# Kernel optimization log

Hardware: AMD Instinct MI355X
Metric: run time of the kernel (lower is better)

The kernel has to match this reference:

```python
import jax, jax.numpy as jnp
import numpy as np

B, T, H = 2, 2048, 1024
I = 4096            # intermediate dim
HEADS = 4
RET = 128           # private expert retrieval dim
NUM_EXPERTS = 4096
NUM_KEYS = 64       # sqrt(NUM_EXPERTS)
K = 8               # num_cdmmoe_experts_per_head


def setup_inputs() -> dict:
    key = jax.random.key(0)
    ks = jax.random.split(key, 7)
    return {
        "hidden_states": jax.random.normal(ks[0], (B, T, H), jnp.float32),
        "W_up": jax.random.normal(ks[1], (I, H), jnp.float32) * 0.02,
        "W_down": jax.random.normal(ks[2], (H, I), jnp.float32) * 0.02,
        "W_q": jax.random.normal(ks[3], (HEADS * RET, H), jnp.float32) * 0.02,
        "keys": jax.random.normal(ks[4], (HEADS, NUM_KEYS, 2, RET // 2), jnp.float32) * 0.02,
        "down_embed": jax.random.normal(ks[5], (NUM_EXPERTS, H), jnp.float32) * 0.02,
        "up_embed": jax.random.normal(ks[6], (NUM_EXPERTS, H), jnp.float32) * 0.02,
    }


def reference(hidden_states, W_up, W_down, W_q, keys, down_embed, up_embed):
    b, t, hd = hidden_states.shape
    h, nk, _, n = keys.shape  # heads, num_keys, 2, half retrieval dim
    # queries: [b,t,h*2n] -> [2,b,t,h,n]
    q = jnp.einsum('btd,ed->bte', hidden_states, W_q)
    q = q.reshape(b, t, 2, h, n).transpose(2, 0, 1, 3, 4)
    # product-key similarities: [2,b,t,h,num_keys]
    sim = jnp.einsum('pbthn,hkpn->pbthk', q, keys)
    scores_xy, idx_xy = jax.lax.top_k(sim, K)  # [2,b,t,h,K]
    sx, sy = scores_xy[0], scores_xy[1]
    ix, iy = idx_xy[0], idx_xy[1]
    # cartesian combine: [b,t,h,K*K]
    all_scores = (sx[..., :, None] + sy[..., None, :]).reshape(b, t, h, K * K)
    all_idx = (ix[..., :, None] * nk + iy[..., None, :]).reshape(b, t, h, K * K)
    scores, pk = jax.lax.top_k(all_scores, K)               # [b,t,h,K]
    indices = jnp.take_along_axis(all_idx, pk, axis=-1)     # [b,t,h,K]
    de = down_embed[indices]  # [b,t,h,K,H]
    ue = up_embed[indices]    # [b,t,h,K,H]
    w = jax.nn.silu(jnp.einsum('btd,bthkd->bthk', hidden_states, de)
                    * jax.nn.softmax(scores, axis=-1))
    experts_states = jnp.einsum('bthk,bthkd->btd', w, ue)
    dense = jnp.einsum('bti,di->btd', jax.nn.silu(jnp.einsum('btd,id->bti', hidden_states, W_up)), W_down)
    return dense + experts_states
```

## Files before the change

### kernel.cpp

```cpp
#include <hip/hip_runtime.h>

typedef unsigned short u16;
typedef unsigned int u32;

#define TOKENS 4096
#define HDIM 1024
#define IDIM 4096
#define NHEADS 4
#define NKEYS 64
#define TOPK 8
#define QDIM 512

typedef __bf16 bf16x8 __attribute__((ext_vector_type(8)));
typedef float  f32x4  __attribute__((ext_vector_type(4)));
typedef u16    u16x8  __attribute__((ext_vector_type(8)));
typedef u16    u16x4  __attribute__((ext_vector_type(4)));
typedef u32    u32x4  __attribute__((ext_vector_type(4)));

__device__ __forceinline__ u16 f2bf(float f) {
    u32 u = __float_as_uint(f);
    u += 0x7fffu + ((u >> 16) & 1u);
    return (u16)(u >> 16);
}
__device__ __forceinline__ float bf2f(u16 h) { return __uint_as_float(((u32)h) << 16); }

#define H_N4   1048576
#define WUP_N4 1048576
#define WDN_N4 1048576
#define DE_N4  1048576
#define UE_N4  1048576
#define CVT_TOT (H_N4 + WUP_N4 + WDN_N4 + DE_N4 + UE_N4)

__device__ __forceinline__ void cvt1(const float* in, u16* hi, u16* lo, int i) {
    float4 v = reinterpret_cast<const float4*>(in)[i];
    float vf[4] = {v.x, v.y, v.z, v.w};
    ushort4 h;
    u16 hh[4];
#pragma unroll
    for (int j = 0; j < 4; j++) hh[j] = f2bf(vf[j]);
    h.x = hh[0]; h.y = hh[1]; h.z = hh[2]; h.w = hh[3];
    reinterpret_cast<ushort4*>(hi)[i] = h;
    if (lo) {
        ushort4 l4;
        u16 ll[4];
#pragma unroll
        for (int j = 0; j < 4; j++) ll[j] = f2bf(vf[j] - bf2f(hh[j]));
        l4.x = ll[0]; l4.y = ll[1]; l4.z = ll[2]; l4.w = ll[3];
        reinterpret_cast<ushort4*>(lo)[i] = l4;
    }
}

__device__ __forceinline__ void cvt1_f8(const float* in, u32* out8, int i) {
    float4 v = reinterpret_cast<const float4*>(in)[i];
    u32 w = __builtin_amdgcn_cvt_pk_fp8_f32(v.x, v.y, 0u, false);
    w = __builtin_amdgcn_cvt_pk_fp8_f32(v.z, v.w, w, true);
    out8[i] = w;
}

__global__ __launch_bounds__(256) void cvt_all(
    const float* __restrict__ hidden, const float* __restrict__ W_up,
    const float* __restrict__ W_down, const float* __restrict__ de,
    const float* __restrict__ ue,
    u16* __restrict__ hid_hi, u16* __restrict__ hid_lo,
    u16* __restrict__ wup, u16* __restrict__ wdn,
    u32* __restrict__ de_f8, u32* __restrict__ ue_f8) {
    int i = blockIdx.x * 256 + threadIdx.x;
    if (i >= CVT_TOT) return;
    if (i < H_N4) { cvt1(hidden, hid_hi, hid_lo, i); return; }
    i -= H_N4;
    if (i < WUP_N4) { cvt1(W_up, wup, nullptr, i); return; }
    i -= WUP_N4;
    if (i < WDN_N4) { cvt1(W_down, wdn, nullptr, i); return; }
    i -= WDN_N4;
    if (i < DE_N4) { cvt1_f8(de, de_f8, i); return; }
    i -= DE_N4;
    cvt1_f8(ue, ue_f8, i);
}

__global__ __launch_bounds__(256) void weff_kernel(
    const float* __restrict__ keys, const float* __restrict__ Wq,
    u16* __restrict__ weff_hi, u16* __restrict__ weff_lo) {
    __shared__ float kk[64][65];
    __shared__ float wq_s[64][128];

    const int g = blockIdx.x >> 3, ds = blockIdx.x & 7;
    const int p = g >> 2, h = g & 3;
    const int d0 = ds * 128;
    const int t = threadIdx.x;
    const int base = p * 256 + h * 64;

    {
        int k = t >> 2, part = t & 3;
        const float* krow = keys + (((size_t)(h * NKEYS + k) * 2 + p) * 64);
#pragma unroll
        for (int j = 0; j < 4; j++) {
            int n0 = part * 16 + j * 4;
            float4 v = *reinterpret_cast<const float4*>(krow + n0);
            kk[k][n0 + 0] = v.x; kk[k][n0 + 1] = v.y;
            kk[k][n0 + 2] = v.z; kk[k][n0 + 3] = v.w;
        }
    }
    {
        int n = t >> 2, dpart = t & 3;
        const float* wrow = Wq + (size_t)(base + n) * HDIM + d0;
#pragma unroll
        for (int j = 0; j < 8; j++) {
            int dd = dpart * 32 + j * 4;
            float4 v = *reinterpret_cast<const float4*>(wrow + dd);
            *reinterpret_cast<float4*>(&wq_s[n][dd]) = v;
        }
    }
    __syncthreads();

    const int k = t & 63, dq = t >> 6;
    float acc[32];
#pragma unroll
    for (int i = 0; i < 32; i++) acc[i] = 0.f;
    for (int n = 0; n < 64; n++) {
        float kv = kk[k][n];
        const float4* wrow = reinterpret_cast<const float4*>(&wq_s[n][dq * 32]);
#pragma unroll
        for (int j = 0; j < 8; j++) {
            float4 w4 = wrow[j];
            acc[j * 4 + 0] += kv * w4.x; acc[j * 4 + 1] += kv * w4.y;
            acc[j * 4 + 2] += kv * w4.z; acc[j * 4 + 3] += kv * w4.w;
        }
    }
    size_t ro = (size_t)(g * 64 + k) * HDIM + d0 + dq * 32;
#pragma unroll
    for (int j = 0; j < 8; j++) {
        ushort4 hh, ll;
        u16 hv[4], lv[4];
#pragma unroll
        for (int i = 0; i < 4; i++) {
            float a = acc[j * 4 + i];
            hv[i] = f2bf(a);
            lv[i] = f2bf(a - bf2f(hv[i]));
        }
        hh.x = hv[0]; hh.y = hv[1]; hh.z = hv[2]; hh.w = hv[3];
        ll.x = lv[0]; ll.y = lv[1]; ll.z = lv[2]; ll.w = lv[3];
        *reinterpret_cast<ushort4*>(weff_hi + ro + j * 4) = hh;
        *reinterpret_cast<ushort4*>(weff_lo + ro + j * 4) = ll;
    }
}

__global__ __launch_bounds__(256) void reduce_add(float* __restrict__ out,
                                                  const float* __restrict__ p, int n4) {
    int i = blockIdx.x * 256 + threadIdx.x;
    if (i >= n4) return;
    float4 a = reinterpret_cast<const float4*>(out)[i];
    float4 b = reinterpret_cast<const float4*>(p)[i];
    a.x += b.x; a.y += b.y; a.z += b.z; a.w += b.w;
    reinterpret_cast<float4*>(out)[i] = a;
}

__device__ __forceinline__ void gload16(const void* g, void* s) {
    auto gp = reinterpret_cast<const __attribute__((address_space(1))) u32*>(
        reinterpret_cast<uintptr_t>(g));
    auto sp = reinterpret_cast<__attribute__((address_space(3))) u32*>(
        reinterpret_cast<uintptr_t>(s));
    __builtin_amdgcn_global_load_lds(gp, sp, 16, 0, 0);
}

#define BK 32

__device__ __forceinline__ int swz(int a) { return a ^ (((a >> 7) & 3) << 4); }

template <int ROWS, int THREADS>
__device__ __forceinline__ void stage_tile(const u16* g, size_t krow_b, size_t kb0,
                                           u16* s, int t) {
#pragma unroll
    for (int rnd = 0; rnd < ROWS * 64 / (THREADS * 16); rnd++) {
        int o = t * 16 + rnd * THREADS * 16;
        int os = swz(o);
        int row = o >> 6, kb = os & 63;
        gload16((const char*)g + (size_t)row * krow_b + kb0 + kb, (char*)s + o);
    }
}

template <int EPI, int TBM, int TBN, int WVM, int WVN, bool SPLIT, int KCHUNKS, bool XSWZ>
__global__ __launch_bounds__(WVM * WVN * 64) void gemm_bt(
    const u16* __restrict__ A, const u16* __restrict__ Alo,
    const u16* __restrict__ B, const u16* __restrict__ Blo,
    void* __restrict__ Cout, void* __restrict__ Cout2,
    const float* __restrict__ ext, int M, int N, int K) {
    constexpr int THREADS = WVM * WVN * 64;
    constexpr int NS = SPLIT ? 2 : 1;
    constexpr int WM = TBM / WVM, WN = TBN / WVN;
    constexpr int FM = WM / 16, FN = WN / 16;
    constexpr int ASZ = NS * TBM * BK;
    constexpr int BSZ = NS * TBN * BK;
    __shared__ u16 As[2][ASZ];
    __shared__ u16 Bs[2][BSZ];
    const int t = threadIdx.x;
    const int lane = t & 63;
    const int wave = t >> 6;
    const int wr = wave / WVN, wc = wave % WVN;

    int bx = blockIdx.x, by = blockIdx.y;
    if (XSWZ) {
        int gx = gridDim.x, gy = gridDim.y;
        int n = gx * gy;
        int bid = by * gx + bx;
        int q = n >> 3;
        bid = (bid & 7) * q + (bid >> 3);
        bx = bid % gx; by = bid / gx;
    }
    const int m0 = by * TBM;
    const int n0 = bx * TBN;
    const int klen = K / KCHUNKS;
    const int koff = (KCHUNKS > 1) ? blockIdx.z * klen : 0;

    f32x4 acc[FM][FN];
#pragma unroll
    for (int i = 0; i < FM; i++)
#pragma unroll
        for (int j = 0; j < FN; j++) acc[i][j] = (f32x4){0.f, 0.f, 0.f, 0.f};

    const size_t krow = (size_t)K * 2;
    const int ro = lane & 15;
    const int ko = (lane >> 4) * 16;

    const u16* Ab = A + (size_t)m0 * K;
    const u16* Bb = B + (size_t)n0 * K;
    const u16* Alb = SPLIT ? Alo + (size_t)m0 * K : nullptr;
    const u16* Blb = SPLIT ? Blo + (size_t)n0 * K : nullptr;

    auto stage_all = [&](int b, int k0) {
        size_t kb0 = (size_t)k0 * 2;
        stage_tile<TBM, THREADS>(Ab, krow, kb0, As[b], t);
        stage_tile<TBN, THREADS>(Bb, krow, kb0, Bs[b], t);
        if (SPLIT) {
            stage_tile<TBM, THREADS>(Alb, krow, kb0, As[b] + TBM * BK, t);
            stage_tile<TBN, THREADS>(Blb, krow, kb0, Bs[b] + TBN * BK, t);
        }
    };

    stage_all(0, koff);
    __syncthreads();
    int cur = 0;

    for (int k0 = koff; k0 < koff + klen; k0 += BK) {
        if (k0 + BK < koff + klen) stage_all(cur ^ 1, k0 + BK);
        const u16* Ac = As[cur];
        const u16* Bc = Bs[cur];
        bf16x8 fa[FM], fb[FN], fal[FM], fbl[FN];
#pragma unroll
        for (int i = 0; i < FM; i++) {
            int a = swz((wr * WM + i * 16 + ro) * 64 + ko);
            fa[i] = *reinterpret_cast<const bf16x8*>((const char*)Ac + a);
            if (SPLIT)
                fal[i] = *reinterpret_cast<const bf16x8*>((const char*)(Ac + TBM * BK) + a);
        }
#pragma unroll
        for (int j = 0; j < FN; j++) {
            int a = swz((wc * WN + j * 16 + ro) * 64 + ko);
            fb[j] = *reinterpret_cast<const bf16x8*>((const char*)Bc + a);
            if (SPLIT)
                fbl[j] = *reinterpret_cast<const bf16x8*>((const char*)(Bc + TBN * BK) + a);
        }
#pragma unroll
        for (int i = 0; i < FM; i++)
#pragma unroll
            for (int j = 0; j < FN; j++) {
                acc[i][j] = __builtin_amdgcn_mfma_f32_16x16x32_bf16(fa[i], fb[j],
                                                                    acc[i][j], 0, 0, 0);
                if (SPLIT) {
                    acc[i][j] = __builtin_amdgcn_mfma_f32_16x16x32_bf16(fa[i], fbl[j],
                                                                        acc[i][j], 0, 0, 0);
                    acc[i][j] = __builtin_amdgcn_mfma_f32_16x16x32_bf16(fal[i], fb[j],
                                                                        acc[i][j], 0, 0, 0);
                }
            }
        __syncthreads();
        cur ^= 1;
    }

#pragma unroll
    for (int i = 0; i < FM; i++)
#pragma unroll
        for (int j = 0; j < FN; j++) {
            int col = n0 + wc * WN + j * 16 + (lane & 15);
            int rbase = m0 + wr * WM + i * 16 + (lane >> 4) * 4;
#pragma unroll
            for (int r = 0; r < 4; r++) {
                int row = rbase + r;
                float v = acc[i][j][r];
                size_t off = (size_t)row * N + col;
                if (EPI == 0) {
                    ((float*)Cout)[off] = v;
                } else if (EPI == 1) {
                    float s = v / (1.f + __expf(-v));
                    ((u16*)Cout)[off] = f2bf(s);
                } else {
                    if (KCHUNKS == 1 || blockIdx.z == 0)
                        ((float*)Cout)[off] = v + ext[off];
                    else
                        ((float*)Cout2)[off] = v;
                }
            }
        }
}

__device__ __forceinline__ int rank64(const float* base, float v, int l) {
    const float4* gv = reinterpret_cast<const float4*>(base);
    int rank = 0;
#pragma unroll
    for (int n = 0; n < 16; n++) {
        float4 o = gv[n];
        int b = n * 4;
        rank += (o.x > v) || (o.x == v && (b + 0) < l);
        rank += (o.y > v) || (o.y == v && (b + 1) < l);
        rank += (o.z > v) || (o.z == v && (b + 2) < l);
        rank += (o.w > v) || (o.w == v && (b + 3) < l);
    }
    return rank;
}

__global__ __launch_bounds__(512) void router(
    const float* __restrict__ Simb,
    int* __restrict__ sidx_g, float* __restrict__ gate_g) {
    __shared__ float sims[QDIM];
    __shared__ float topv[8][TOPK];
    __shared__ int topi[8][TOPK];
    __shared__ float pv[NHEADS][64];
    __shared__ float st8[NHEADS][TOPK];
    __shared__ int sid8[NHEADS][TOPK];

    const int tok = blockIdx.x;
    const int tid = threadIdx.x;
    const int w = tid >> 6, l = tid & 63;

    sims[tid] = Simb[(size_t)tok * QDIM + tid];
    __syncthreads();

    {
        float v = sims[w * 64 + l];
        int rank = rank64(sims + w * 64, v, l);
        if (rank < TOPK) { topv[w][rank] = v; topi[w][rank] = l; }
    }
    __syncthreads();

    if (w < NHEADS) {
        pv[w][l] = topv[w][l >> 3] + topv[4 + w][l & 7];
    }
    __syncthreads();

    if (w < NHEADS) {
        float v = pv[w][l];
        int rank = rank64(pv[w], v, l);
        if (rank < TOPK) {
            st8[w][rank] = v;
            sid8[w][rank] = topi[w][l >> 3] * NKEYS + topi[4 + w][l & 7];
        }
    }
    __syncthreads();

    if (tid < NHEADS * TOPK) {
        int h = tid >> 3, r = tid & 7;
        float m0 = st8[h][0];
        float s = 0.f;
#pragma unroll
        for (int i = 0; i < TOPK; i++) s += __expf(st8[h][i] - m0);
        size_t o = ((size_t)tok * NHEADS + h) * TOPK + r;
        sidx_g[o] = sid8[h][r];
        gate_g[o] = __expf(st8[h][r] - m0) / s;
    }
}

__global__ __launch_bounds__(256) void expert_gather(
    const u16* __restrict__ hid_bf, const u32* __restrict__ de_f8,
    const u32* __restrict__ ue_f8, const int* __restrict__ sidx_g,
    const float* __restrict__ gate_g, float* __restrict__ expst) {
    __shared__ float wks[32];
    __shared__ int eids_s[32];

    const int tok = blockIdx.x;
    const int w = threadIdx.x >> 6, l = threadIdx.x & 63;

    {
        u16x8 hv[2];
        const u16* hrow = hid_bf + (size_t)tok * HDIM + l * 16;
        hv[0] = *reinterpret_cast<const u16x8*>(hrow);
        hv[1] = *reinterpret_cast<const u16x8*>(hrow + 8);
        float h16[16];
#pragma unroll
        for (int t2 = 0; t2 < 8; t2++) { h16[t2] = bf2f(hv[0][t2]); h16[8 + t2] = bf2f(hv[1][t2]); }
        int eid[8];
        float gt[8];
#pragma unroll
        for (int j = 0; j < 8; j++) {
            size_t o = (size_t)tok * 32 + w * 8 + j;
            eid[j] = sidx_g[o];
            gt[j] = gate_g[o];
        }
        u32x4 dv[8];
#pragma unroll
        for (int j = 0; j < 8; j++) {
            const u32x4* dr = reinterpret_cast<const u32x4*>(de_f8 + (size_t)eid[j] * 256 + l * 4);
            dv[j] = *dr;
        }
        float dot[8];
#pragma unroll
        for (int j = 0; j < 8; j++) {
            float s = 0.f;
#pragma unroll
            for (int w2 = 0; w2 < 4; w2++) {
                u32 word = dv[j][w2];
                s += h16[w2 * 4 + 0] * __builtin_amdgcn_cvt_f32_fp8(word, 0);
                s += h16[w2 * 4 + 1] * __builtin_amdgcn_cvt_f32_fp8(word, 1);
                s += h16[w2 * 4 + 2] * __builtin_amdgcn_cvt_f32_fp8(word, 2);
                s += h16[w2 * 4 + 3] * __builtin_amdgcn_cvt_f32_fp8(word, 3);
            }
            dot[j] = s;
        }
#pragma unroll
        for (int m = 32; m; m >>= 1)
#pragma unroll
            for (int j = 0; j < 8; j++) dot[j] += __shfl_xor(dot[j], m, 64);
#pragma unroll
        for (int j = 0; j < 8; j++)
            if (l == j) {
                float x = dot[j] * gt[j];
                wks[w * 8 + j] = x / (1.f + __expf(-x));
                eids_s[w * 8 + j] = eid[j];
            }
    }
    __syncthreads();

    {
        float acc0 = 0.f, acc1 = 0.f, acc2 = 0.f, acc3 = 0.f;
        const u32* ubase = ue_f8 + w * 64 + l;
#pragma unroll
        for (int m = 0; m < 32; m++) {
            int e = eids_s[m];
            float wk = wks[m];
            u32 u = ubase[(size_t)e * 256];
            acc0 += wk * __builtin_amdgcn_cvt_f32_fp8(u, 0);
            acc1 += wk * __builtin_amdgcn_cvt_f32_fp8(u, 1);
            acc2 += wk * __builtin_amdgcn_cvt_f32_fp8(u, 2);
            acc3 += wk * __builtin_amdgcn_cvt_f32_fp8(u, 3);
        }
        float4 a4 = make_float4(acc0, acc1, acc2, acc3);
        *reinterpret_cast<float4*>(expst + (size_t)tok * HDIM + w * 256 + l * 4) = a4;
    }
}

extern "C" void kernel_launch(void* const* d_in, const int* in_sizes, int n_in,
                              void* d_out, int out_size, void* d_ws, size_t ws_size,
                              hipStream_t stream) {
    const float* hidden = (const float*)d_in[0];
    const float* W_up = (const float*)d_in[1];
    const float* W_down = (const float*)d_in[2];
    const float* W_q = (const float*)d_in[3];
    const float* keys = (const float*)d_in[4];
    const float* down_embed = (const float*)d_in[5];
    const float* up_embed = (const float*)d_in[6];
    float* out = (float*)d_out;

    char* ws = (char*)d_ws;
    size_t off = 0;
    auto alloc = [&](size_t bytes) {
        void* p = ws + off;
        off += (bytes + 255) & ~(size_t)255;
        return p;
    };
    u16* hid_hi = (u16*)alloc((size_t)TOKENS * HDIM * 2);
    u16* hid_lo = (u16*)alloc((size_t)TOKENS * HDIM * 2);
    float* Simb = (float*)alloc((size_t)TOKENS * QDIM * 4);
    float* partial = (float*)hid_lo;
    u16* weff_hi = (u16*)alloc((size_t)QDIM * HDIM * 2);
    u16* weff_lo = (u16*)alloc((size_t)QDIM * HDIM * 2);
    u16* wup = (u16*)alloc((size_t)IDIM * HDIM * 2);
    u16* wdn = (u16*)alloc((size_t)HDIM * IDIM * 2);
    u16* act = (u16*)alloc((size_t)TOKENS * IDIM * 2);
    u32* de_f8 = (u32*)alloc((size_t)4096 * HDIM);
    u32* ue_f8 = (u32*)alloc((size_t)4096 * HDIM);
    float* expst = (float*)alloc((size_t)TOKENS * HDIM * 4);
    int* sidx_g = (int*)alloc((size_t)TOKENS * 32 * 4);
    float* gate_g = (float*)alloc((size_t)TOKENS * 32 * 4);

    cvt_all<<<(CVT_TOT + 255) / 256, 256, 0, stream>>>(
        hidden, W_up, W_down, down_embed, up_embed,
        hid_hi, hid_lo, wup, wdn, de_f8, ue_f8);
    weff_kernel<<<64, 256, 0, stream>>>(keys, W_q, weff_hi, weff_lo);

    gemm_bt<0, 64, 128, 2, 2, true, 1, false>
        <<<dim3(QDIM / 128, TOKENS / 64), 256, 0, stream>>>(
        hid_hi, hid_lo, weff_hi, weff_lo, Simb, nullptr, nullptr, TOKENS, QDIM, HDIM);

    router<<<TOKENS, 512, 0, stream>>>(Simb, sidx_g, gate_g);
    expert_gather<<<TOKENS, 256, 0, stream>>>(hid_hi, de_f8, ue_f8, sidx_g, gate_g, expst);

    gemm_bt<1, 256, 128, 4, 2, false, 1, true>
        <<<dim3(IDIM / 128, TOKENS / 256), 512, 0, stream>>>(
        hid_hi, nullptr, wup, nullptr, act, nullptr, nullptr, TOKENS, IDIM, HDIM);
    gemm_bt<2, 128, 128, 2, 2, false, 2, true>
        <<<dim3(HDIM / 128, TOKENS / 128, 2), 256, 0, stream>>>(
        act, nullptr, wdn, nullptr, out, partial, expst, TOKENS, HDIM, IDIM);
    reduce_add<<<(TOKENS * HDIM / 4 + 255) / 256, 256, 0, stream>>>(out, partial,
                                                                    TOKENS * HDIM / 4);
}
```

Measured before the change: 222.7 us.

## Add 256x256-tile pipelined GEMM for dense MLP with four-way split-K down projection

Replaces the generic GEMM used for the dense up and down projections with a dedicated 512-thread kernel. It uses 256x256 output tiles and a K-step of 64, and splits each K-step into four quadrant phases that interleave direct-to-LDS loads with MFMA, using manual waitcnt, barriers and setprio. The down projection is split four ways along K; the partial sums go to reused workspace buffers, and a three-input reduction kernel adds them into the output. The goal is more data reuse per tile and better overlap of loads with compute. In exchange the kernel needs more registers (one block per CU), and correctness depends on aliasing partial buffers onto workspace that is dead by that point.

```diff
diff --git a/kernel.cpp b/kernel.cpp
--- a/kernel.cpp
+++ b/kernel.cpp
@@ -144,13 +144,18 @@
     }
 }
 
-__global__ __launch_bounds__(256) void reduce_add(float* __restrict__ out,
-                                                  const float* __restrict__ p, int n4) {
+__global__ __launch_bounds__(256) void reduce_add3(float* __restrict__ out,
+                                                   const float* __restrict__ p1,
+                                                   const float* __restrict__ p2,
+                                                   const float* __restrict__ p3, int n4) {
     int i = blockIdx.x * 256 + threadIdx.x;
     if (i >= n4) return;
     float4 a = reinterpret_cast<const float4*>(out)[i];
-    float4 b = reinterpret_cast<const float4*>(p)[i];
-    a.x += b.x; a.y += b.y; a.z += b.z; a.w += b.w;
+    float4 b = reinterpret_cast<const float4*>(p1)[i];
+    float4 c = reinterpret_cast<const float4*>(p2)[i];
+    float4 d = reinterpret_cast<const float4*>(p3)[i];
+    a.x += b.x + c.x + d.x; a.y += b.y + c.y + d.y;
+    a.z += b.z + c.z + d.z; a.w += b.w + c.w + d.w;
     reinterpret_cast<float4*>(out)[i] = a;
 }
 
@@ -178,12 +183,11 @@
     }
 }
 
-template <int EPI, int TBM, int TBN, int WVM, int WVN, bool SPLIT, int KCHUNKS, bool XSWZ>
+template <int EPI, int TBM, int TBN, int WVM, int WVN, bool SPLIT>
 __global__ __launch_bounds__(WVM * WVN * 64) void gemm_bt(
     const u16* __restrict__ A, const u16* __restrict__ Alo,
     const u16* __restrict__ B, const u16* __restrict__ Blo,
-    void* __restrict__ Cout, void* __restrict__ Cout2,
-    const float* __restrict__ ext, int M, int N, int K) {
+    void* __restrict__ Cout, int M, int N, int K) {
     constexpr int THREADS = WVM * WVN * 64;
     constexpr int NS = SPLIT ? 2 : 1;
     constexpr int WM = TBM / WVM, WN = TBN / WVN;
@@ -196,20 +200,8 @@
     const int lane = t & 63;
     const int wave = t >> 6;
     const int wr = wave / WVN, wc = wave % WVN;
-
-    int bx = blockIdx.x, by = blockIdx.y;
-    if (XSWZ) {
-        int gx = gridDim.x, gy = gridDim.y;
-        int n = gx * gy;
-        int bid = by * gx + bx;
-        int q = n >> 3;
-        bid = (bid & 7) * q + (bid >> 3);
-        bx = bid % gx; by = bid / gx;
-    }
-    const int m0 = by * TBM;
-    const int n0 = bx * TBN;
-    const int klen = K / KCHUNKS;
-    const int koff = (KCHUNKS > 1) ? blockIdx.z * klen : 0;
+    const int m0 = blockIdx.y * TBM;
+    const int n0 = blockIdx.x * TBN;
 
     f32x4 acc[FM][FN];
 #pragma unroll
@@ -236,12 +228,12 @@
         }
     };
 
-    stage_all(0, koff);
+    stage_all(0, 0);
     __syncthreads();
     int cur = 0;
 
-    for (int k0 = koff; k0 < koff + klen; k0 += BK) {
-        if (k0 + BK < koff + klen) stage_all(cur ^ 1, k0 + BK);
+    for (int k0 = 0; k0 < K; k0 += BK) {
+        if (k0 + BK < K) stage_all(cur ^ 1, k0 + BK);
         const u16* Ac = As[cur];
         const u16* Bc = Bs[cur];
         bf16x8 fa[FM], fb[FN], fal[FM], fbl[FN];
@@ -284,22 +276,151 @@
             int rbase = m0 + wr * WM + i * 16 + (lane >> 4) * 4;
 #pragma unroll
             for (int r = 0; r < 4; r++) {
-                int row = rbase + r;
-                float v = acc[i][j][r];
-                size_t off = (size_t)row * N + col;
-                if (EPI == 0) {
-                    ((float*)Cout)[off] = v;
-                } else if (EPI == 1) {
+                size_t off = (size_t)(rbase + r) * N + col;
+                ((float*)Cout)[off] = acc[i][j][r];
+            }
+        }
+}
+
+template <int EPI, int KCHUNKS>
+__global__ __launch_bounds__(512, 1) void gemm8(
+    const u16* __restrict__ A, const u16* __restrict__ B,
+    void* __restrict__ Cout,
+    float* __restrict__ P1, float* __restrict__ P2, float* __restrict__ P3,
+    const float* __restrict__ ext, int M, int N, int K) {
+    __shared__ u16 As[2][2][128 * 64];
+    __shared__ u16 Bs[2][2][128 * 64];
+    const int t = threadIdx.x;
+    const int lane = t & 63;
+    const int wave = t >> 6;
+    const int wr = wave >> 2, wc = wave & 3;
+    const int ro = lane & 15;
+    const int ko = (lane >> 4) * 16;
+
+    int bx = blockIdx.x, by = blockIdx.y;
+    {
+        int gx = gridDim.x;
+        int n = gx * gridDim.y;
+        int bid = by * gx + bx;
+        int q = n >> 3;
+        bid = (bid & 7) * q + (bid >> 3);
+        bx = bid % gx; by = bid / gx;
+    }
+    const int m0 = by * 256, n0 = bx * 256;
+    const int klen = K / KCHUNKS;
+    const int z = (KCHUNKS > 1) ? blockIdx.z : 0;
+    const int koff = z * klen;
+    const int NT = klen / 64;
+
+    const size_t krowB = (size_t)K * 2;
+    const u16* A0p = A + (size_t)m0 * K;
+    const u16* A1p = A + (size_t)(m0 + 128) * K;
+    const u16* B0p = B + (size_t)n0 * K;
+    const u16* B1p = B + (size_t)(n0 + 128) * K;
+
+    f32x4 acc[8][4];
+#pragma unroll
+    for (int i = 0; i < 8; i++)
+#pragma unroll
+        for (int j = 0; j < 4; j++) acc[i][j] = (f32x4){0.f, 0.f, 0.f, 0.f};
+
+    auto stage = [&](const u16* gbase, int kelem, u16* lds) {
+#pragma unroll
+        for (int rnd = 0; rnd < 2; rnd++) {
+            int o = t * 16 + rnd * 8192;
+            int os = o ^ (((o >> 7) & 7) << 4);
+            int row = o >> 7, kb = os & 127;
+            gload16((const char*)gbase + (size_t)row * krowB + (size_t)kelem * 2 + kb,
+                    (char*)lds + o);
+        }
+    };
+
+    stage(A0p, koff, As[0][0]);
+    stage(B0p, koff, Bs[0][0]);
+    stage(B1p, koff, Bs[0][1]);
+    stage(A1p, koff, As[0][1]);
+    stage(A0p, koff + 64, As[1][0]);
+    stage(B0p, koff + 64, Bs[1][0]);
+    asm volatile("s_waitcnt vmcnt(4)" ::: "memory");
+    asm volatile("s_barrier" ::: "memory");
+
+#define PHASE(R)                                                               \
+    {                                                                          \
+        const int qm = (R) >> 1, qn = (R) & 1;                                 \
+        const u16* Ah = As[u & 1][qm];                                         \
+        const u16* Bh = Bs[u & 1][qn];                                         \
+        bf16x8 fa[4][2], fb[2][2];                                             \
+        _Pragma("unroll") for (int i = 0; i < 4; i++) {                        \
+            int hr = wr * 64 + i * 16 + ro;                                    \
+            int sw = (hr & 7) << 4;                                            \
+            _Pragma("unroll") for (int kk = 0; kk < 2; kk++)                   \
+                fa[i][kk] = *reinterpret_cast<const bf16x8*>(                  \
+                    (const char*)Ah + ((hr * 128 + kk * 64 + ko) ^ sw));       \
+        }                                                                      \
+        _Pragma("unroll") for (int j = 0; j < 2; j++) {                        \
+            int hr = wc * 32 + j * 16 + ro;                                    \
+            int sw = (hr & 7) << 4;                                            \
+            _Pragma("unroll") for (int kk = 0; kk < 2; kk++)                   \
+                fb[j][kk] = *reinterpret_cast<const bf16x8*>(                  \
+                    (const char*)Bh + ((hr * 128 + kk * 64 + ko) ^ sw));       \
+        }                                                                      \
+        if ((R) == 0 && u + 1 < NT) stage(B1p, koff + (u + 1) * 64, Bs[(u + 1) & 1][1]); \
+        if ((R) == 1 && u + 1 < NT) stage(A1p, koff + (u + 1) * 64, As[(u + 1) & 1][1]); \
+        if ((R) == 2 && u + 2 < NT) stage(A0p, koff + (u + 2) * 64, As[u & 1][0]);       \
+        if ((R) == 3 && u + 2 < NT) stage(B0p, koff + (u + 2) * 64, Bs[u & 1][0]);       \
+        asm volatile("s_barrier" ::: "memory");                                \
+        __builtin_amdgcn_s_setprio(1);                                         \
+        _Pragma("unroll") for (int i = 0; i < 4; i++)                          \
+            _Pragma("unroll") for (int j = 0; j < 2; j++)                      \
+                _Pragma("unroll") for (int kk = 0; kk < 2; kk++)               \
+                    acc[qm * 4 + i][qn * 2 + j] =                              \
+                        __builtin_amdgcn_mfma_f32_16x16x32_bf16(               \
+                            fa[i][kk], fb[j][kk], acc[qm * 4 + i][qn * 2 + j], \
+                            0, 0, 0);                                          \
+        __builtin_amdgcn_s_setprio(0);                                         \
+        if ((R) == 3) {                                                        \
+            if (u == NT - 2)                                                   \
+                asm volatile("s_waitcnt vmcnt(0)" ::: "memory");               \
+            else                                                               \
+                asm volatile("s_waitcnt vmcnt(4)" ::: "memory");               \
+        }                                                                      \
+        asm volatile("s_barrier" ::: "memory");                                \
+    }
+
+    for (int u = 0; u < NT; ++u) {
+        PHASE(0)
+        PHASE(1)
+        PHASE(2)
+        PHASE(3)
+    }
+#undef PHASE
+
+#pragma unroll
+    for (int qi = 0; qi < 8; qi++) {
+#pragma unroll
+        for (int qj = 0; qj < 4; qj++) {
+            const int qm = qi >> 2, i = qi & 3;
+            const int qn = qj >> 1, j = qj & 1;
+            int row0 = m0 + qm * 128 + wr * 64 + i * 16 + (lane >> 4) * 4;
+            int col = n0 + qn * 128 + wc * 32 + j * 16 + ro;
+#pragma unroll
+            for (int r = 0; r < 4; r++) {
+                float v = acc[qi][qj][r];
+                size_t off = (size_t)(row0 + r) * N + col;
+                if (EPI == 1) {
                     float s = v / (1.f + __expf(-v));
                     ((u16*)Cout)[off] = f2bf(s);
                 } else {
-                    if (KCHUNKS == 1 || blockIdx.z == 0)
+                    if (z == 0)
                         ((float*)Cout)[off] = v + ext[off];
-                    else
-                        ((float*)Cout2)[off] = v;
+                    else {
+                        float* P = (z == 1) ? P1 : (z == 2) ? P2 : P3;
+                        P[off] = v;
+                    }
                 }
             }
         }
+    }
 }
 
 __device__ __forceinline__ int rank64(const float* base, float v, int l) {
@@ -468,7 +589,6 @@
     u16* hid_hi = (u16*)alloc((size_t)TOKENS * HDIM * 2);
     u16* hid_lo = (u16*)alloc((size_t)TOKENS * HDIM * 2);
     float* Simb = (float*)alloc((size_t)TOKENS * QDIM * 4);
-    float* partial = (float*)hid_lo;
     u16* weff_hi = (u16*)alloc((size_t)QDIM * HDIM * 2);
     u16* weff_lo = (u16*)alloc((size_t)QDIM * HDIM * 2);
     u16* wup = (u16*)alloc((size_t)IDIM * HDIM * 2);
@@ -479,25 +599,26 @@
     float* expst = (float*)alloc((size_t)TOKENS * HDIM * 4);
     int* sidx_g = (int*)alloc((size_t)TOKENS * 32 * 4);
     float* gate_g = (float*)alloc((size_t)TOKENS * 32 * 4);
+    float* P3 = (float*)alloc((size_t)TOKENS * HDIM * 4);
+    float* P1 = (float*)hid_hi;
+    float* P2 = (float*)Simb;
 
     cvt_all<<<(CVT_TOT + 255) / 256, 256, 0, stream>>>(
         hidden, W_up, W_down, down_embed, up_embed,
         hid_hi, hid_lo, wup, wdn, de_f8, ue_f8);
     weff_kernel<<<64, 256, 0, stream>>>(keys, W_q, weff_hi, weff_lo);
 
-    gemm_bt<0, 64, 128, 2, 2, true, 1, false>
+    gemm_bt<0, 64, 128, 2, 2, true>
         <<<dim3(QDIM / 128, TOKENS / 64), 256, 0, stream>>>(
-        hid_hi, hid_lo, weff_hi, weff_lo, Simb, nullptr, nullptr, TOKENS, QDIM, HDIM);
+        hid_hi, hid_lo, weff_hi, weff_lo, Simb, TOKENS, QDIM, HDIM);
 
     router<<<TOKENS, 512, 0, stream>>>(Simb, sidx_g, gate_g);
     expert_gather<<<TOKENS, 256, 0, stream>>>(hid_hi, de_f8, ue_f8, sidx_g, gate_g, expst);
 
-    gemm_bt<1, 256, 128, 4, 2, false, 1, true>
-        <<<dim3(IDIM / 128, TOKENS / 256), 512, 0, stream>>>(
-        hid_hi, nullptr, wup, nullptr, act, nullptr, nullptr, TOKENS, IDIM, HDIM);
-    gemm_bt<2, 128, 128, 2, 2, false, 2, true>
-        <<<dim3(HDIM / 128, TOKENS / 128, 2), 256, 0, stream>>>(
-        act, nullptr, wdn, nullptr, out, partial, expst, TOKENS, HDIM, IDIM);
-    reduce_add<<<(TOKENS * HDIM / 4 + 255) / 256, 256, 0, stream>>>(out, partial,
-                                                                    TOKENS * HDIM / 4);
-}
+    gemm8<1, 1><<<dim3(IDIM / 256, TOKENS / 256), 512, 0, stream>>>(
+        hid_hi, wup, act, nullptr, nullptr, nullptr, nullptr, TOKENS, IDIM, HDIM);
+    gemm8<2, 4><<<dim3(HDIM / 256, TOKENS / 256, 4), 512, 0, stream>>>(
+        act, wdn, out, P1, P2, P3, expst, TOKENS, HDIM, IDIM);
+    reduce_add3<<<(TOKENS * HDIM / 4 + 255) / 256, 256, 0, stream>>>(
+        out, P1, P2, P3, TOKENS * HDIM / 4);
+}
```

Result: slower. 246.3 us (+10.6%).

## Add triple-buffered GEMM with explicit vmcnt waits for dense up/down projections

Applied to the files above, without the earlier changes.

Introduces a new gemm_p3 kernel for the two dense MLP GEMMs that uses three LDS stages, prefetching two K-tiles ahead. It waits on outstanding global loads with explicit s_waitcnt vmcnt counts and raw s_barrier instead of __syncthreads. The aim is to hide global-load latency behind MFMA work. The cost is more shared memory per block, which may lower occupancy, and the hand-counted vmcnt values assume each staging call issues exactly LPS loads. The original gemm_bt is reduced to the router GEMM path.

```diff
diff --git a/kernel.cpp b/kernel.cpp
--- a/kernel.cpp
+++ b/kernel.cpp
@@ -178,12 +178,22 @@
     }
 }
 
-template <int EPI, int TBM, int TBN, int WVM, int WVN, bool SPLIT, int KCHUNKS, bool XSWZ>
+template <int N>
+__device__ __forceinline__ void vm_wait() {
+    if constexpr (N == 0) asm volatile("s_waitcnt vmcnt(0)" ::: "memory");
+    else if constexpr (N == 2) asm volatile("s_waitcnt vmcnt(2)" ::: "memory");
+    else if constexpr (N == 3) asm volatile("s_waitcnt vmcnt(3)" ::: "memory");
+    else if constexpr (N == 4) asm volatile("s_waitcnt vmcnt(4)" ::: "memory");
+    else if constexpr (N == 6) asm volatile("s_waitcnt vmcnt(6)" ::: "memory");
+    else if constexpr (N == 8) asm volatile("s_waitcnt vmcnt(8)" ::: "memory");
+    else static_assert(N == 0, "unsupported vmcnt");
+}
+
+template <int EPI, int TBM, int TBN, int WVM, int WVN, bool SPLIT>
 __global__ __launch_bounds__(WVM * WVN * 64) void gemm_bt(
     const u16* __restrict__ A, const u16* __restrict__ Alo,
     const u16* __restrict__ B, const u16* __restrict__ Blo,
-    void* __restrict__ Cout, void* __restrict__ Cout2,
-    const float* __restrict__ ext, int M, int N, int K) {
+    void* __restrict__ Cout, int M, int N, int K) {
     constexpr int THREADS = WVM * WVN * 64;
     constexpr int NS = SPLIT ? 2 : 1;
     constexpr int WM = TBM / WVM, WN = TBN / WVN;
@@ -196,20 +206,8 @@
     const int lane = t & 63;
     const int wave = t >> 6;
     const int wr = wave / WVN, wc = wave % WVN;
-
-    int bx = blockIdx.x, by = blockIdx.y;
-    if (XSWZ) {
-        int gx = gridDim.x, gy = gridDim.y;
-        int n = gx * gy;
-        int bid = by * gx + bx;
-        int q = n >> 3;
-        bid = (bid & 7) * q + (bid >> 3);
-        bx = bid % gx; by = bid / gx;
-    }
-    const int m0 = by * TBM;
-    const int n0 = bx * TBN;
-    const int klen = K / KCHUNKS;
-    const int koff = (KCHUNKS > 1) ? blockIdx.z * klen : 0;
+    const int m0 = blockIdx.y * TBM;
+    const int n0 = blockIdx.x * TBN;
 
     f32x4 acc[FM][FN];
 #pragma unroll
@@ -236,12 +234,12 @@
         }
     };
 
-    stage_all(0, koff);
+    stage_all(0, 0);
     __syncthreads();
     int cur = 0;
 
-    for (int k0 = koff; k0 < koff + klen; k0 += BK) {
-        if (k0 + BK < koff + klen) stage_all(cur ^ 1, k0 + BK);
+    for (int k0 = 0; k0 < K; k0 += BK) {
+        if (k0 + BK < K) stage_all(cur ^ 1, k0 + BK);
         const u16* Ac = As[cur];
         const u16* Bc = Bs[cur];
         bf16x8 fa[FM], fb[FN], fal[FM], fbl[FN];
@@ -284,16 +282,113 @@
             int rbase = m0 + wr * WM + i * 16 + (lane >> 4) * 4;
 #pragma unroll
             for (int r = 0; r < 4; r++) {
-                int row = rbase + r;
+                size_t off = (size_t)(rbase + r) * N + col;
+                ((float*)Cout)[off] = acc[i][j][r];
+            }
+        }
+}
+
+template <int EPI, int TBM, int TBN, int WVM, int WVN, int KCHUNKS, bool XSWZ>
+__global__ __launch_bounds__(WVM * WVN * 64) void gemm_p3(
+    const u16* __restrict__ A, const u16* __restrict__ B,
+    void* __restrict__ Cout, void* __restrict__ Cout2,
+    const float* __restrict__ ext, int M, int N, int K) {
+    constexpr int THREADS = WVM * WVN * 64;
+    constexpr int WM = TBM / WVM, WN = TBN / WVN;
+    constexpr int FM = WM / 16, FN = WN / 16;
+    constexpr int LPS = (TBM + TBN) * 64 / (THREADS * 16);
+    __shared__ u16 As[3][TBM * BK];
+    __shared__ u16 Bs[3][TBN * BK];
+    const int t = threadIdx.x;
+    const int lane = t & 63;
+    const int wave = t >> 6;
+    const int wr = wave / WVN, wc = wave % WVN;
+    const int ro = lane & 15;
+    const int ko = (lane >> 4) * 16;
+
+    int bx = blockIdx.x, by = blockIdx.y;
+    if (XSWZ) {
+        int gx = gridDim.x;
+        int n = gx * gridDim.y;
+        int bid = by * gx + bx;
+        int q = n >> 3;
+        bid = (bid & 7) * q + (bid >> 3);
+        bx = bid % gx; by = bid / gx;
+    }
+    const int m0 = by * TBM;
+    const int n0 = bx * TBN;
+    const int klen = K / KCHUNKS;
+    const int z = (KCHUNKS > 1) ? blockIdx.z : 0;
+    const int koff = z * klen;
+    const int NU = klen / BK;
+
+    f32x4 acc[FM][FN];
+#pragma unroll
+    for (int i = 0; i < FM; i++)
+#pragma unroll
+        for (int j = 0; j < FN; j++) acc[i][j] = (f32x4){0.f, 0.f, 0.f, 0.f};
+
+    const size_t krow = (size_t)K * 2;
+    const u16* Ab = A + (size_t)m0 * K;
+    const u16* Bb = B + (size_t)n0 * K;
+
+    auto stage_all = [&](int b, int k0) {
+        size_t kb0 = (size_t)k0 * 2;
+        stage_tile<TBM, THREADS>(Ab, krow, kb0, As[b], t);
+        stage_tile<TBN, THREADS>(Bb, krow, kb0, Bs[b], t);
+    };
+
+    stage_all(0, koff);
+    stage_all(1, koff + BK);
+
+    int cur = 0, pre = 2;
+    for (int u = 0; u < NU; ++u) {
+        int k0 = koff + u * BK;
+        if (u + 2 < NU) stage_all(pre, k0 + 2 * BK);
+        if (u + 2 < NU) vm_wait<2 * LPS>();
+        else if (u + 1 < NU) vm_wait<LPS>();
+        else vm_wait<0>();
+        __builtin_amdgcn_s_barrier();
+
+        const u16* Ac = As[cur];
+        const u16* Bc = Bs[cur];
+        bf16x8 fa[FM], fb[FN];
+#pragma unroll
+        for (int i = 0; i < FM; i++) {
+            int a = swz((wr * WM + i * 16 + ro) * 64 + ko);
+            fa[i] = *reinterpret_cast<const bf16x8*>((const char*)Ac + a);
+        }
+#pragma unroll
+        for (int j = 0; j < FN; j++) {
+            int a = swz((wc * WN + j * 16 + ro) * 64 + ko);
+            fb[j] = *reinterpret_cast<const bf16x8*>((const char*)Bc + a);
+        }
+#pragma unroll
+        for (int i = 0; i < FM; i++)
+#pragma unroll
+            for (int j = 0; j < FN; j++)
+                acc[i][j] = __builtin_amdgcn_mfma_f32_16x16x32_bf16(fa[i], fb[j],
+                                                                    acc[i][j], 0, 0, 0);
+        __builtin_amdgcn_s_barrier();
+        cur = (cur == 2) ? 0 : cur + 1;
+        pre = (pre == 2) ? 0 : pre + 1;
+    }
+
+#pragma unroll
+    for (int i = 0; i < FM; i++)
+#pragma unroll
+        for (int j = 0; j < FN; j++) {
+            int col = n0 + wc * WN + j * 16 + ro;
+            int rbase = m0 + wr * WM + i * 16 + (lane >> 4) * 4;
+#pragma unroll
+            for (int r = 0; r < 4; r++) {
                 float v = acc[i][j][r];
-                size_t off = (size_t)row * N + col;
-                if (EPI == 0) {
-                    ((float*)Cout)[off] = v;
-                } else if (EPI == 1) {
+                size_t off = (size_t)(rbase + r) * N + col;
+                if (EPI == 1) {
                     float s = v / (1.f + __expf(-v));
                     ((u16*)Cout)[off] = f2bf(s);
                 } else {
-                    if (KCHUNKS == 1 || blockIdx.z == 0)
+                    if (KCHUNKS == 1 || z == 0)
                         ((float*)Cout)[off] = v + ext[off];
                     else
                         ((float*)Cout2)[off] = v;
@@ -485,19 +580,19 @@
         hid_hi, hid_lo, wup, wdn, de_f8, ue_f8);
     weff_kernel<<<64, 256, 0, stream>>>(keys, W_q, weff_hi, weff_lo);
 
-    gemm_bt<0, 64, 128, 2, 2, true, 1, false>
+    gemm_bt<0, 64, 128, 2, 2, true>
         <<<dim3(QDIM / 128, TOKENS / 64), 256, 0, stream>>>(
-        hid_hi, hid_lo, weff_hi, weff_lo, Simb, nullptr, nullptr, TOKENS, QDIM, HDIM);
+        hid_hi, hid_lo, weff_hi, weff_lo, Simb, TOKENS, QDIM, HDIM);
 
     router<<<TOKENS, 512, 0, stream>>>(Simb, sidx_g, gate_g);
     expert_gather<<<TOKENS, 256, 0, stream>>>(hid_hi, de_f8, ue_f8, sidx_g, gate_g, expst);
 
-    gemm_bt<1, 256, 128, 4, 2, false, 1, true>
+    gemm_p3<1, 256, 128, 4, 2, 1, true>
         <<<dim3(IDIM / 128, TOKENS / 256), 512, 0, stream>>>(
-        hid_hi, nullptr, wup, nullptr, act, nullptr, nullptr, TOKENS, IDIM, HDIM);
-    gemm_bt<2, 128, 128, 2, 2, false, 2, true>
+        hid_hi, wup, act, nullptr, nullptr, TOKENS, IDIM, HDIM);
+    gemm_p3<2, 128, 128, 2, 2, 2, true>
         <<<dim3(HDIM / 128, TOKENS / 128, 2), 256, 0, stream>>>(
-        act, nullptr, wdn, nullptr, out, partial, expst, TOKENS, HDIM, IDIM);
+        act, wdn, out, partial, expst, TOKENS, HDIM, IDIM);
     reduce_add<<<(TOKENS * HDIM / 4 + 255) / 256, 256, 0, stream>>>(out, partial,
                                                                     TOKENS * HDIM / 4);
 }
```

Measured after the change: 217.0 us. -2.6%, faster.
